# Kernel tuning notes

Measured on AMD Instinct MI355X. Metric: run time of the kernel, lower is better.

Reference implementation:

```python
import jax, jax.numpy as jnp
import numpy as np
import math

B, C, H, W = 4, 256, 56, 56
RC = 32  # max(256 // 8, 8)
EPS = 1e-5


def _conv(x, w, pad):
    return jax.lax.conv_general_dilated(
        x, w, window_strides=(1, 1), padding=[(pad, pad), (pad, pad)],
        dimension_numbers=('NCHW', 'OIHW', 'NCHW'))


def setup_inputs() -> dict:
    key = jax.random.key(0)
    ks = jax.random.split(key, 9)
    s = 0.05  # keep attention logits in a sane range
    return {
        'x': jax.random.normal(ks[0], (B, C, H, W), jnp.float32),
        'wq1': jax.random.normal(ks[1], (RC, C, 1, 1), jnp.float32) * s,
        'wq3': jax.random.normal(ks[2], (RC, C, 3, 3), jnp.float32) * s,
        'wq5': jax.random.normal(ks[3], (RC, C, 5, 5), jnp.float32) * s,
        'wq7': jax.random.normal(ks[4], (RC, C, 7, 7), jnp.float32) * s,
        'wk': jax.random.normal(ks[5], (RC, C, 1, 1), jnp.float32) * s,
        'wv': jax.random.normal(ks[6], (C, C, 1, 1), jnp.float32) * s,
        'wproj': jax.random.normal(ks[7], (C, 4 * C, 1, 1), jnp.float32) * s,
        'gamma': jnp.ones((C,), jnp.float32),
        'beta': jnp.zeros((C,), jnp.float32),
    }


def reference(x, wq1, wq3, wq5, wq7, wk, wv, wproj, gamma, beta):
    b, c, h, w = x.shape
    hw = h * w
    scale = 1.0 / math.sqrt(RC)
    k = _conv(x, wk, 0).reshape(b, RC, hw)   # [B, RC, HW]
    v = _conv(x, wv, 0).reshape(b, c, hw)    # [B, C, HW]
    attended = []
    for wq, pad in ((wq1, 0), (wq3, 1), (wq5, 2), (wq7, 3)):
        q = _conv(x, wq, pad).reshape(b, RC, hw)          # [B, RC, HW]
        scores = jnp.einsum('bri,brj->bij', q, k) * scale  # [B, HW, HW]
        attn = jax.nn.softmax(scores, axis=-1)
        att = jnp.einsum('bcj,bij->bci', v, attn)          # [B, C, HW]
        attended.append(att.reshape(b, c, h, w))
    concat = jnp.concatenate(attended, axis=1)             # [B, 4C, H, W]
    out = _conv(concat, wproj, 0) + x                      # residual before BN
    # BatchNorm2d in training mode: batch stats (biased var), affine
    mean = out.mean(axis=(0, 2, 3), keepdims=True)
    var = out.var(axis=(0, 2, 3), keepdims=True)
    out = (out - mean) * jax.lax.rsqrt(var + EPS)
    return out * gamma[None, :, None, None] + beta[None, :, None, None]
```

## Files before the change

### kernel.cpp

```cpp
#include <hip/hip_runtime.h>
#include <hip/hip_bf16.h>
#include <math.h>

#define HW 3136
#define WIDTH 56
#define CC 256
#define BB 4
#define RCH 32
#define NJT (HW / 64)
#define SCLOG2E 0.2550437041556575f

using bf16x8 = __attribute__((ext_vector_type(8))) short;
using f32x4  = __attribute__((ext_vector_type(4))) float;

static __device__ __forceinline__ unsigned short f2bf(float f) {
    __hip_bfloat16 h = __float2bfloat16(f);
    return *reinterpret_cast<unsigned short*>(&h);
}

__global__ __launch_bounds__(256) void prep_weights(
    const float* __restrict__ wq3, const float* __restrict__ wq5,
    const float* __restrict__ wq7, const float* __restrict__ wproj,
    const float* __restrict__ wk, const float* __restrict__ wq1,
    const float* __restrict__ wv,
    unsigned short* __restrict__ Wb3, unsigned short* __restrict__ Wb5,
    unsigned short* __restrict__ Wb7, unsigned short* __restrict__ Wpb,
    unsigned short* __restrict__ Wkq, unsigned short* __restrict__ Wvb) {
    int e = blockIdx.x * 256 + threadIdx.x;
    if (e < 73728) {
        int c = e & 255, r = (e >> 8) & 31, t = e >> 13;
        Wb3[e] = f2bf(wq3[((size_t)r * 256 + c) * 9 + t]);
    } else if (e < 278528) {
        int i = e - 73728;
        int c = i & 255, r = (i >> 8) & 31, t = i >> 13;
        Wb5[i] = f2bf(wq5[((size_t)r * 256 + c) * 25 + t]);
    } else if (e < 679936) {
        int i = e - 278528;
        int c = i & 255, r = (i >> 8) & 31, t = i >> 13;
        Wb7[i] = f2bf(wq7[((size_t)r * 256 + c) * 49 + t]);
    } else if (e < 942080) {
        int i = e - 679936;
        Wpb[i] = f2bf(wproj[i]);
    } else if (e < 958464) {
        int i = e - 942080;
        Wkq[i] = f2bf(i < 8192 ? wk[i] : wq1[i - 8192]);
    } else if (e < 1024000) {
        int i = e - 958464;
        Wvb[i] = f2bf(wv[i]);
    }
}

__global__ __launch_bounds__(256) void transpose_x(
    const float* __restrict__ x, unsigned short* __restrict__ xT) {
    __shared__ unsigned short tile[32][33];
    const int b = blockIdx.z;
    const int i0 = blockIdx.x * 32, c0 = blockIdx.y * 32;
    const int tx = threadIdx.x & 31, ty = threadIdx.x >> 5;
    #pragma unroll
    for (int k = 0; k < 4; ++k)
        tile[ty + k * 8][tx] = f2bf(x[((size_t)b * CC + c0 + ty + k * 8) * HW + i0 + tx]);
    __syncthreads();
    #pragma unroll
    for (int k = 0; k < 4; ++k)
        xT[((size_t)b * HW + i0 + ty + k * 8) * 256 + c0 + tx] = tile[tx][ty + k * 8];
}

__global__ __launch_bounds__(256) void qk32_mfma(
    const unsigned short* __restrict__ xT, const unsigned short* __restrict__ Wkq,
    unsigned short* __restrict__ Kt, unsigned short* __restrict__ Qt) {
    const int b = blockIdx.y, z = blockIdx.z;
    const int i0 = blockIdx.x * 64;
    const int t = threadIdx.x;
    const int lane = t & 63, w = t >> 6, lg = lane >> 4, li = lane & 15;

    unsigned short* outp = z == 0 ? Kt : Qt;
    const float osc = z == 0 ? 1.0f : SCLOG2E;
    const unsigned short* wb = Wkq + z * 8192;
    const unsigned short* xb = xT + ((size_t)b * HW + i0 + w * 16 + li) * 256;

    const f32x4 z4 = (f32x4){0.f, 0.f, 0.f, 0.f};
    f32x4 acc[2] = {z4, z4};

    for (int c0 = 0; c0 < 256; c0 += 32) {
        bf16x8 ax = *(const bf16x8*)(xb + c0 + lg * 8);
        #pragma unroll
        for (int rs = 0; rs < 2; ++rs) {
            bf16x8 bw = *(const bf16x8*)(wb + (size_t)(rs * 16 + li) * 256 + c0 + lg * 8);
            acc[rs] = __builtin_amdgcn_mfma_f32_16x16x32_bf16(ax, bw, acc[rs], 0, 0, 0);
        }
    }
    unsigned short* qb = outp + ((size_t)b * HW + i0 + w * 16 + lg * 4) * 32;
    #pragma unroll
    for (int rs = 0; rs < 2; ++rs)
        #pragma unroll
        for (int r = 0; r < 4; ++r)
            qb[(size_t)r * 32 + rs * 16 + li] = f2bf(acc[rs][r] * osc);
}

__global__ __launch_bounds__(256) void v_mfma(
    const unsigned short* __restrict__ xT, const unsigned short* __restrict__ Wvb,
    unsigned short* __restrict__ Vb) {
    const int b = blockIdx.y;
    const int i0 = blockIdx.x * 32;
    const int t = threadIdx.x;
    const int lane = t & 63, w = t >> 6, lg = lane >> 4, li = lane & 15;

    const f32x4 z4 = (f32x4){0.f, 0.f, 0.f, 0.f};
    f32x4 acc[4][2];
    #pragma unroll
    for (int ct = 0; ct < 4; ++ct) { acc[ct][0] = z4; acc[ct][1] = z4; }

    const unsigned short* xb = xT + (size_t)b * HW * 256;

    for (int c0 = 0; c0 < 256; c0 += 32) {
        bf16x8 bx[2];
        #pragma unroll
        for (int is = 0; is < 2; ++is)
            bx[is] = *(const bf16x8*)(xb + (size_t)(i0 + is * 16 + li) * 256 + c0 + lg * 8);
        #pragma unroll
        for (int ct = 0; ct < 4; ++ct) {
            bf16x8 aw = *(const bf16x8*)(
                Wvb + (size_t)(w * 64 + ct * 16 + li) * 256 + c0 + lg * 8);
            #pragma unroll
            for (int is = 0; is < 2; ++is)
                acc[ct][is] = __builtin_amdgcn_mfma_f32_16x16x32_bf16(
                    aw, bx[is], acc[ct][is], 0, 0, 0);
        }
    }
    #pragma unroll
    for (int ct = 0; ct < 4; ++ct)
        #pragma unroll
        for (int is = 0; is < 2; ++is)
            #pragma unroll
            for (int r = 0; r < 4; ++r)
                Vb[((size_t)b * CC + w * 64 + ct * 16 + lg * 4 + r) * HW +
                   i0 + is * 16 + li] = f2bf(acc[ct][is][r]);
}

template <int KS>
static __device__ __forceinline__ void qconv_body(
    const unsigned short* __restrict__ xT,
    const unsigned short* __restrict__ Wb,
    unsigned short* __restrict__ q,
    unsigned short (*xs)[40]) {
    constexpr int P = (KS - 1) / 2;
    constexpr int KT = KS * KS;
    constexpr int ROWS = 64 + 114 * P;
    const int b = blockIdx.y;
    const int i0 = blockIdx.x * 64;
    const int t = threadIdx.x;
    const int lane = t & 63;
    const int w = t >> 6;
    const int li = lane & 15;
    const int lg = lane >> 4;

    const int base = i0 - P * 57;
    const int mycol = (i0 + w * 16 + li) % WIDTH;

    f32x4 acc[2];
    acc[0] = (f32x4){0.f, 0.f, 0.f, 0.f};
    acc[1] = (f32x4){0.f, 0.f, 0.f, 0.f};

    const unsigned short* xTb = xT + (size_t)b * HW * 256;

    for (int c0 = 0; c0 < 256; c0 += 32) {
        __syncthreads();
        for (int e = t; e < ROWS * 4; e += 256) {
            int row = e >> 2, cs = e & 3;
            int gidx = base + row;
            uint4 val = make_uint4(0, 0, 0, 0);
            if (gidx >= 0 && gidx < HW)
                val = *(const uint4*)(xTb + (size_t)gidx * 256 + c0 + cs * 8);
            *(uint4*)(&xs[row][cs * 8]) = val;
        }
        __syncthreads();

        #pragma unroll
        for (int tap = 0; tap < KT; ++tap) {
            const int dx = tap % KS - P;
            const int poff = (tap / KS) * WIDTH + tap % KS;
            bf16x8 a = *(const bf16x8*)(&xs[w * 16 + li + poff][lg * 8]);
            if ((unsigned)(mycol + dx) >= (unsigned)WIDTH)
                a = (bf16x8){0, 0, 0, 0, 0, 0, 0, 0};
            const unsigned short* wrow =
                Wb + (size_t)tap * 32 * 256 + c0 + lg * 8;
            bf16x8 b0 = *(const bf16x8*)(wrow + (size_t)li * 256);
            bf16x8 b1 = *(const bf16x8*)(wrow + (size_t)(16 + li) * 256);
            acc[0] = __builtin_amdgcn_mfma_f32_16x16x32_bf16(a, b0, acc[0], 0, 0, 0);
            acc[1] = __builtin_amdgcn_mfma_f32_16x16x32_bf16(a, b1, acc[1], 0, 0, 0);
        }
    }

    unsigned short* qb = q + ((size_t)b * HW + i0 + w * 16 + lg * 4) * 32;
    #pragma unroll
    for (int rs = 0; rs < 2; ++rs)
        #pragma unroll
        for (int r = 0; r < 4; ++r)
            qb[(size_t)r * 32 + rs * 16 + li] = f2bf(acc[rs][r] * SCLOG2E);
}

__global__ __launch_bounds__(256) void qconv_all(
    const unsigned short* __restrict__ xT,
    const unsigned short* __restrict__ Wb3,
    const unsigned short* __restrict__ Wb5,
    const unsigned short* __restrict__ Wb7,
    unsigned short* __restrict__ Qt) {
    __shared__ unsigned short xs[406][40];
    const size_t QSLICE = (size_t)BB * HW * 32;
    if (blockIdx.z == 0)      qconv_body<3>(xT, Wb3, Qt + 1 * QSLICE, xs);
    else if (blockIdx.z == 1) qconv_body<5>(xT, Wb5, Qt + 2 * QSLICE, xs);
    else                      qconv_body<7>(xT, Wb7, Qt + 3 * QSLICE, xs);
}

__global__ __launch_bounds__(256) void flashmfma(
    const unsigned short* __restrict__ Qt, const unsigned short* __restrict__ Kt,
    const unsigned short* __restrict__ Vb, unsigned short* __restrict__ ATTb) {
    const int b = blockIdx.y, g = blockIdx.z;
    const int i0 = blockIdx.x * 64;
    const int t = threadIdx.x;
    const int lane = t & 63;
    const int w = t >> 6;
    const int lg = lane >> 4;
    const int li = lane & 15;

    __shared__ __align__(16) unsigned short Ps[64][72];
    __shared__ float lls[64];

    const bf16x8 aq = *(const bf16x8*)(
        Qt + ((size_t)(g * BB + b) * HW + i0 + w * 16 + li) * 32 + lg * 8);

    const f32x4 z4 = (f32x4){0.f, 0.f, 0.f, 0.f};
    f32x4 acc[4][4];
    #pragma unroll
    for (int ct = 0; ct < 4; ++ct)
        #pragma unroll
        for (int is = 0; is < 4; ++is) acc[ct][is] = z4;

    float lsum[4] = {0.f, 0.f, 0.f, 0.f};

    const unsigned short* Kb = Kt + (size_t)b * HW * 32;
    const unsigned short* Vw = Vb + ((size_t)b * CC + w * 64) * HW;

    for (int jt = 0; jt < NJT; ++jt) {
        const int j0 = jt * 64;

        f32x4 S[4];
        #pragma unroll
        for (int j2 = 0; j2 < 4; ++j2) {
            bf16x8 bk = *(const bf16x8*)(Kb + (size_t)(j0 + j2 * 16 + li) * 32 + lg * 8);
            S[j2] = __builtin_amdgcn_mfma_f32_16x16x32_bf16(aq, bk, z4, 0, 0, 0);
        }

        unsigned int pk0[4], pk1[4];
        #pragma unroll
        for (int r = 0; r < 4; ++r) {
            float p0 = __builtin_amdgcn_exp2f(S[0][r]);
            float p1 = __builtin_amdgcn_exp2f(S[1][r]);
            float p2 = __builtin_amdgcn_exp2f(S[2][r]);
            float p3 = __builtin_amdgcn_exp2f(S[3][r]);
            lsum[r] += (p0 + p1) + (p2 + p3);
            asm("v_cvt_pk_bf16_f32 %0, %1, %2" : "=v"(pk0[r]) : "v"(p0), "v"(p1));
            asm("v_cvt_pk_bf16_f32 %0, %1, %2" : "=v"(pk1[r]) : "v"(p2), "v"(p3));
        }

        __syncthreads();
        #pragma unroll
        for (int r = 0; r < 4; ++r) {
            const int row = w * 16 + lg * 4 + r;
            Ps[row][li]      = (unsigned short)pk0[r];
            Ps[row][16 + li] = (unsigned short)(pk0[r] >> 16);
            Ps[row][32 + li] = (unsigned short)pk1[r];
            Ps[row][48 + li] = (unsigned short)(pk1[r] >> 16);
        }
        __syncthreads();

        bf16x8 bp[4][2];
        #pragma unroll
        for (int is = 0; is < 4; ++is)
            #pragma unroll
            for (int ks = 0; ks < 2; ++ks)
                bp[is][ks] = *(const bf16x8*)(&Ps[is * 16 + li][ks * 32 + lg * 8]);

        #pragma unroll
        for (int ct = 0; ct < 4; ++ct) {
            #pragma unroll
            for (int ks = 0; ks < 2; ++ks) {
                bf16x8 av = *(const bf16x8*)(
                    Vw + (size_t)(ct * 16 + li) * HW + j0 + ks * 32 + lg * 8);
                #pragma unroll
                for (int is = 0; is < 4; ++is)
                    acc[ct][is] = __builtin_amdgcn_mfma_f32_16x16x32_bf16(
                        av, bp[is][ks], acc[ct][is], 0, 0, 0);
            }
        }
    }

    #pragma unroll
    for (int r = 0; r < 4; ++r) {
        float s = lsum[r];
        #pragma unroll
        for (int off = 1; off < 16; off <<= 1) s += __shfl_xor(s, off);
        if (li == 0) lls[w * 16 + lg * 4 + r] = s;
    }
    __syncthreads();

    float invl[4];
    #pragma unroll
    for (int is = 0; is < 4; ++is) invl[is] = 1.f / lls[is * 16 + li];

    #pragma unroll
    for (int ct = 0; ct < 4; ++ct)
        #pragma unroll
        for (int is = 0; is < 4; ++is)
            #pragma unroll
            for (int r = 0; r < 4; ++r) {
                int c = w * 64 + ct * 16 + lg * 4 + r;
                ATTb[((size_t)b * (4 * CC) + g * CC + c) * HW + i0 + is * 16 + li] =
                    f2bf(acc[ct][is][r] * invl[is]);
            }
}

__global__ __launch_bounds__(256) void gemm_proj(
    const unsigned short* __restrict__ ATTb, const unsigned short* __restrict__ Wpb,
    const float* __restrict__ x, float* __restrict__ out) {
    const int b = blockIdx.y;
    const int i0 = blockIdx.x * 32;
    const int t = threadIdx.x;
    const int lane = t & 63;
    const int w = t >> 6;
    const int lg = lane >> 4;
    const int li = lane & 15;

    __shared__ __align__(16) unsigned short As[32][72];

    const f32x4 z4 = (f32x4){0.f, 0.f, 0.f, 0.f};
    f32x4 acc[4][2];
    #pragma unroll
    for (int ct = 0; ct < 4; ++ct) { acc[ct][0] = z4; acc[ct][1] = z4; }

    for (int k0 = 0; k0 < 1024; k0 += 64) {
        __syncthreads();
        {
            int row = t >> 2, seg = t & 3;
            uint4 v = *(const uint4*)(
                ATTb + ((size_t)b * 1024 + k0 + row) * HW + i0 + seg * 8);
            const unsigned short* sv = (const unsigned short*)&v;
            #pragma unroll
            for (int u = 0; u < 8; ++u) As[seg * 8 + u][row] = sv[u];
        }
        __syncthreads();

        #pragma unroll
        for (int k2 = 0; k2 < 2; ++k2) {
            bf16x8 afr[2];
            #pragma unroll
            for (int is = 0; is < 2; ++is)
                afr[is] = *(const bf16x8*)(&As[is * 16 + li][k2 * 32 + lg * 8]);
            #pragma unroll
            for (int ct = 0; ct < 4; ++ct) {
                bf16x8 wf = *(const bf16x8*)(
                    Wpb + (size_t)(w * 64 + ct * 16 + li) * 1024 + k0 + k2 * 32 + lg * 8);
                #pragma unroll
                for (int is = 0; is < 2; ++is)
                    acc[ct][is] = __builtin_amdgcn_mfma_f32_16x16x32_bf16(
                        wf, afr[is], acc[ct][is], 0, 0, 0);
            }
        }
    }

    #pragma unroll
    for (int ct = 0; ct < 4; ++ct)
        #pragma unroll
        for (int is = 0; is < 2; ++is)
            #pragma unroll
            for (int r = 0; r < 4; ++r) {
                int co = w * 64 + ct * 16 + lg * 4 + r;
                size_t o = ((size_t)b * CC + co) * HW + i0 + is * 16 + li;
                out[o] = acc[ct][is][r] + x[o];
            }
}

__global__ __launch_bounds__(256) void bnstats(
    const float* __restrict__ out, float* __restrict__ mean,
    float* __restrict__ rstd) {
    const int c = blockIdx.x;
    float s = 0.f, s2 = 0.f;
    for (int e = threadIdx.x; e < BB * HW; e += 256) {
        int b = e / HW, i = e - b * HW;
        float v = out[((size_t)b * CC + c) * HW + i];
        s += v; s2 += v * v;
    }
    __shared__ float rs[256], rs2[256];
    rs[threadIdx.x] = s; rs2[threadIdx.x] = s2;
    __syncthreads();
    for (int st = 128; st > 0; st >>= 1) {
        if (threadIdx.x < st) {
            rs[threadIdx.x] += rs[threadIdx.x + st];
            rs2[threadIdx.x] += rs2[threadIdx.x + st];
        }
        __syncthreads();
    }
    if (threadIdx.x == 0) {
        const float n = (float)(BB * HW);
        float m = rs[0] / n;
        float var = rs2[0] / n - m * m;
        mean[c] = m;
        rstd[c] = rsqrtf(var + 1e-5f);
    }
}

__global__ __launch_bounds__(256) void bnapply(
    float* __restrict__ out, const float* __restrict__ mean,
    const float* __restrict__ rstd, const float* __restrict__ gamma,
    const float* __restrict__ beta) {
    size_t idx = (size_t)blockIdx.x * 256 + threadIdx.x;
    if (idx < (size_t)BB * CC * HW) {
        int c = (int)((idx / HW) % CC);
        out[idx] = (out[idx] - mean[c]) * rstd[c] * gamma[c] + beta[c];
    }
}

extern "C" void kernel_launch(void* const* d_in, const int* in_sizes, int n_in,
                              void* d_out, int out_size, void* d_ws, size_t ws_size,
                              hipStream_t stream) {
    const float* x     = (const float*)d_in[0];
    const float* wq1   = (const float*)d_in[1];
    const float* wq3   = (const float*)d_in[2];
    const float* wq5   = (const float*)d_in[3];
    const float* wq7   = (const float*)d_in[4];
    const float* wk    = (const float*)d_in[5];
    const float* wv    = (const float*)d_in[6];
    const float* wproj = (const float*)d_in[7];
    const float* gamma = (const float*)d_in[8];
    const float* beta  = (const float*)d_in[9];
    float* out = (float*)d_out;

    unsigned short* ATTb = (unsigned short*)d_ws;
    unsigned short* Kt   = ATTb + (size_t)BB * 4 * CC * HW;
    unsigned short* Qt   = Kt + (size_t)BB * HW * 32;
    unsigned short* Vb   = Qt + (size_t)4 * BB * HW * 32;
    unsigned short* xT   = Vb + (size_t)BB * CC * HW;
    unsigned short* Wb3  = xT + (size_t)BB * HW * CC;
    unsigned short* Wb5  = Wb3 + (size_t)9 * 32 * 256;
    unsigned short* Wb7  = Wb5 + (size_t)25 * 32 * 256;
    unsigned short* Wpb  = Wb7 + (size_t)49 * 32 * 256;
    unsigned short* Wkq  = Wpb + (size_t)256 * 1024;
    unsigned short* Wvb  = Wkq + (size_t)2 * 32 * 256;
    float* mean = (float*)(Wvb + (size_t)256 * 256);
    float* rstd = mean + CC;

    dim3 blk(256);

    prep_weights<<<dim3(4000), blk, 0, stream>>>(
        wq3, wq5, wq7, wproj, wk, wq1, wv, Wb3, Wb5, Wb7, Wpb, Wkq, Wvb);
    transpose_x<<<dim3(HW / 32, CC / 32, BB), blk, 0, stream>>>(x, xT);

    qk32_mfma<<<dim3(HW / 64, BB, 2), blk, 0, stream>>>(xT, Wkq, Kt, Qt);
    v_mfma<<<dim3(HW / 32, BB), blk, 0, stream>>>(xT, Wvb, Vb);

    qconv_all<<<dim3(HW / 64, BB, 3), blk, 0, stream>>>(xT, Wb3, Wb5, Wb7, Qt);

    flashmfma<<<dim3(HW / 64, BB, 4), blk, 0, stream>>>(Qt, Kt, Vb, ATTb);

    gemm_proj<<<dim3(HW / 32, BB), blk, 0, stream>>>(ATTb, Wpb, x, out);

    bnstats<<<dim3(CC), blk, 0, stream>>>(out, mean, rstd);
    bnapply<<<dim3((BB * CC * HW + 255) / 256), blk, 0, stream>>>(out, mean, rstd, gamma, beta);
}
```

Before: 494.8 us.

## Compute scores transposed per wave to keep P in registers, drop LDS staging

Each wave now computes the full 64x64 score tile itself with K as the A operand, so the exp'd probabilities land in the register layout the PV MFMA needs as its B operand. This removes the shared-memory P buffer, both __syncthreads per tile, and the LDS row-sum reduction. V loads are split into two 8-byte pieces to match the permuted k ordering. The cost is that QK^T work is done four times (once per wave) along with four times the exp2 work, plus more registers held for bq and wds.

Result: slower. 703.5 us (+42.2%).

```diff
diff --git a/kernel.cpp b/kernel.cpp
--- a/kernel.cpp
+++ b/kernel.cpp
@@ -223,13 +223,14 @@
     const int lg = lane >> 4;
     const int li = lane & 15;
 
-    __shared__ __align__(16) unsigned short Ps[64][72];
-    __shared__ float lls[64];
-
-    const bf16x8 aq = *(const bf16x8*)(
-        Qt + ((size_t)(g * BB + b) * HW + i0 + w * 16 + li) * 32 + lg * 8);
-
     const f32x4 z4 = (f32x4){0.f, 0.f, 0.f, 0.f};
+
+    bf16x8 bq[4];
+    #pragma unroll
+    for (int is = 0; is < 4; ++is)
+        bq[is] = *(const bf16x8*)(
+            Qt + ((size_t)(g * BB + b) * HW + i0 + is * 16 + li) * 32 + lg * 8);
+
     f32x4 acc[4][4];
     #pragma unroll
     for (int ct = 0; ct < 4; ++ct)
@@ -244,69 +245,60 @@
     for (int jt = 0; jt < NJT; ++jt) {
         const int j0 = jt * 64;
 
-        f32x4 S[4];
-        #pragma unroll
-        for (int j2 = 0; j2 < 4; ++j2) {
-            bf16x8 bk = *(const bf16x8*)(Kb + (size_t)(j0 + j2 * 16 + li) * 32 + lg * 8);
-            S[j2] = __builtin_amdgcn_mfma_f32_16x16x32_bf16(aq, bk, z4, 0, 0, 0);
-        }
-
-        unsigned int pk0[4], pk1[4];
-        #pragma unroll
-        for (int r = 0; r < 4; ++r) {
-            float p0 = __builtin_amdgcn_exp2f(S[0][r]);
-            float p1 = __builtin_amdgcn_exp2f(S[1][r]);
-            float p2 = __builtin_amdgcn_exp2f(S[2][r]);
-            float p3 = __builtin_amdgcn_exp2f(S[3][r]);
-            lsum[r] += (p0 + p1) + (p2 + p3);
-            asm("v_cvt_pk_bf16_f32 %0, %1, %2" : "=v"(pk0[r]) : "v"(p0), "v"(p1));
-            asm("v_cvt_pk_bf16_f32 %0, %1, %2" : "=v"(pk1[r]) : "v"(p2), "v"(p3));
-        }
-
-        __syncthreads();
-        #pragma unroll
-        for (int r = 0; r < 4; ++r) {
-            const int row = w * 16 + lg * 4 + r;
-            Ps[row][li]      = (unsigned short)pk0[r];
-            Ps[row][16 + li] = (unsigned short)(pk0[r] >> 16);
-            Ps[row][32 + li] = (unsigned short)pk1[r];
-            Ps[row][48 + li] = (unsigned short)(pk1[r] >> 16);
-        }
-        __syncthreads();
-
-        bf16x8 bp[4][2];
-        #pragma unroll
-        for (int is = 0; is < 4; ++is)
-            #pragma unroll
-            for (int ks = 0; ks < 2; ++ks)
-                bp[is][ks] = *(const bf16x8*)(&Ps[is * 16 + li][ks * 32 + lg * 8]);
+        bf16x8 bk[4];
+        #pragma unroll
+        for (int j2 = 0; j2 < 4; ++j2)
+            bk[j2] = *(const bf16x8*)(Kb + (size_t)(j0 + j2 * 16 + li) * 32 + lg * 8);
+
+        unsigned int wds[4][8];
+        #pragma unroll
+        for (int is = 0; is < 4; ++is) {
+            f32x4 S[4];
+            #pragma unroll
+            for (int j2 = 0; j2 < 4; ++j2)
+                S[j2] = __builtin_amdgcn_mfma_f32_16x16x32_bf16(bk[j2], bq[is], z4, 0, 0, 0);
+            #pragma unroll
+            for (int j2 = 0; j2 < 4; ++j2) {
+                float p0 = __builtin_amdgcn_exp2f(S[j2][0]);
+                float p1 = __builtin_amdgcn_exp2f(S[j2][1]);
+                float p2 = __builtin_amdgcn_exp2f(S[j2][2]);
+                float p3 = __builtin_amdgcn_exp2f(S[j2][3]);
+                lsum[is] += (p0 + p1) + (p2 + p3);
+                asm("v_cvt_pk_bf16_f32 %0, %1, %2" : "=v"(wds[is][2 * j2]) : "v"(p0), "v"(p1));
+                asm("v_cvt_pk_bf16_f32 %0, %1, %2" : "=v"(wds[is][2 * j2 + 1]) : "v"(p2), "v"(p3));
+            }
+        }
 
         #pragma unroll
         for (int ct = 0; ct < 4; ++ct) {
+            const unsigned short* vr = Vw + (size_t)(ct * 16 + li) * HW + j0;
             #pragma unroll
             for (int ks = 0; ks < 2; ++ks) {
-                bf16x8 av = *(const bf16x8*)(
-                    Vw + (size_t)(ct * 16 + li) * HW + j0 + ks * 32 + lg * 8);
+                union { uint2 d2[2]; bf16x8 v; } va;
+                va.d2[0] = *(const uint2*)(vr + ks * 32 + lg * 4);
+                va.d2[1] = *(const uint2*)(vr + ks * 32 + 16 + lg * 4);
                 #pragma unroll
-                for (int is = 0; is < 4; ++is)
+                for (int is = 0; is < 4; ++is) {
+                    union { unsigned int u[4]; bf16x8 v; } pb;
+                    pb.u[0] = wds[is][4 * ks + 0];
+                    pb.u[1] = wds[is][4 * ks + 1];
+                    pb.u[2] = wds[is][4 * ks + 2];
+                    pb.u[3] = wds[is][4 * ks + 3];
                     acc[ct][is] = __builtin_amdgcn_mfma_f32_16x16x32_bf16(
-                        av, bp[is][ks], acc[ct][is], 0, 0, 0);
+                        va.v, pb.v, acc[ct][is], 0, 0, 0);
+                }
             }
         }
     }
 
-    #pragma unroll
-    for (int r = 0; r < 4; ++r) {
-        float s = lsum[r];
-        #pragma unroll
-        for (int off = 1; off < 16; off <<= 1) s += __shfl_xor(s, off);
-        if (li == 0) lls[w * 16 + lg * 4 + r] = s;
-    }
-    __syncthreads();
-
     float invl[4];
     #pragma unroll
-    for (int is = 0; is < 4; ++is) invl[is] = 1.f / lls[is * 16 + li];
+    for (int is = 0; is < 4; ++is) {
+        float s = lsum[is];
+        s += __shfl_xor(s, 16);
+        s += __shfl_xor(s, 32);
+        invl[is] = 1.f / s;
+    }
 
     #pragma unroll
     for (int ct = 0; ct < 4; ++ct)
```
